# Performance work log

Hardware: AMD Instinct MI355X
Metric: run time of the kernel (lower is better)

## Reference

```python
import jax, jax.numpy as jnp
import numpy as np

E, D, H, T = 8, 1024, 2048, 2048  # num_expert, d_model, d_hidden, tokens

def setup_inputs() -> dict:
    key = jax.random.key(0)
    ks = jax.random.split(key, 7)
    return {
        "moe_inp": jax.random.normal(ks[0], (T, D), jnp.float32),
        "Wg": jax.random.normal(ks[1], (D, E), jnp.float32) * 0.02,
        "bg": jnp.zeros((E,), jnp.float32),
        "W1": jax.random.normal(ks[2], (E, D, H), jnp.float32) * 0.02,
        "b1": jnp.zeros((E, H), jnp.float32),
        "W2": jax.random.normal(ks[3], (E, H, D), jnp.float32) * 0.02,
        "b2": jnp.zeros((E, D), jnp.float32),
        "top_k": 2,
    }

def reference(moe_inp, Wg, bg, W1, b1, W2, b2, top_k):
    # NaiveGate: linear gate, top-k select, softmax over the selected logits
    logits = moe_inp @ Wg + bg                      # [T, E]
    top_vals, top_idx = jax.lax.top_k(logits, top_k)  # [T, k]
    gate_score = jax.nn.softmax(top_vals, axis=-1)    # [T, k]

    # Exact (no capacity drop) MoE: scan over experts, mask-combine.
    # Equivalent math to scatter -> per-expert FFN -> gather -> bmm(gate_score, ...).
    def body(acc, xs):
        e, w1, bb1, w2, bb2 = xs
        h = jax.nn.gelu(moe_inp @ w1 + bb1)          # [T, H]
        y = h @ w2 + bb2                             # [T, D]
        w = jnp.sum(jnp.where(top_idx == e, gate_score, 0.0), axis=-1)  # [T]
        return acc + w[:, None] * y, None

    init = jnp.zeros_like(moe_inp)
    xs = (jnp.arange(E), W1, b1, W2, b2)
    moe_outp, _ = jax.lax.scan(body, init, xs)
    return moe_outp, top_idx
```

## Files before the change

### kernel.cpp

```cpp
#include <hip/hip_runtime.h>
#include <stdint.h>

#define T_TOK 2048
#define D_DIM 1024
#define H_DIM 2048
#define N_EXP 8
#define MAXS  4608

#define WS_CNT    0
#define WS_BTOK   256
#define WS_BW     (WS_BTOK + N_EXP*2048*4)
#define WS_XG     (WS_BW + N_EXP*2048*4)
#define WS_HBUF   (WS_XG + (size_t)MAXS*1024*2)
#define WS_W1T    (WS_HBUF + (size_t)MAXS*2048*2)
#define WS_W2T    (WS_W1T + (size_t)N_EXP*1024*2048*2)

typedef __bf16 bf16x8 __attribute__((ext_vector_type(8)));
typedef float  f32x4  __attribute__((ext_vector_type(4)));

__device__ __forceinline__ unsigned short f2bf(float f) {
  unsigned int u = __float_as_uint(f);
  u += 0x7fffu + ((u >> 16) & 1u);
  return (unsigned short)(u >> 16);
}

__device__ __forceinline__ float gelu_tanh(float x) {
  const float u = 0.7978845608028654f * (x + 0.044715f * x * x * x);
  const float t = __expf(-2.0f * fabsf(u));
  const float th = (1.0f - t) * __builtin_amdgcn_rcpf(1.0f + t);
  return 0.5f * x * (1.0f + copysignf(th, u));
}


__device__ __forceinline__ void transpose_body(const float* __restrict__ in,
                                               unsigned short* __restrict__ out,
                                               int Rout, int Cin, int tx, int ty,
                                               void* smem_) {
  float (*tile)[68] = (float (*)[68])smem_;
  const int c0 = tx * 64, r0 = ty * 64;
  const int tid = threadIdx.x;
#pragma unroll
  for (int p = 0; p < 4; ++p) {
    const int idx = p * 256 + tid;
    const int r = idx >> 4, c4 = idx & 15;
    *(float4*)&tile[r][c4 * 4] = *(const float4*)(in + (size_t)(r0 + r) * Cin + c0 + c4 * 4);
  }
  __syncthreads();
#pragma unroll
  for (int p = 0; p < 2; ++p) {
    const int idx = p * 256 + tid;
    const int oc = idx >> 3, seg = idx & 7;
    unsigned u[4];
#pragma unroll
    for (int j = 0; j < 4; ++j) {
      const unsigned lo = f2bf(tile[seg * 8 + 2 * j][oc]);
      const unsigned hi = f2bf(tile[seg * 8 + 2 * j + 1][oc]);
      u[j] = lo | (hi << 16);
    }
    *(uint4*)(out + (size_t)(c0 + oc) * Rout + r0 + seg * 8) = make_uint4(u[0], u[1], u[2], u[3]);
  }
}

__device__ __forceinline__ void gate_body(int t, const float* __restrict__ x,
                                          const float* __restrict__ Wg,
                                          const float* __restrict__ bg,
                                          float* __restrict__ out_idx,
                                          int* __restrict__ cnt, int* __restrict__ btok,
                                          float* __restrict__ bw) {
  const int lane = threadIdx.x & 63;
  float p[8];
#pragma unroll
  for (int i = 0; i < 8; ++i) p[i] = 0.f;
  const float* xr = x + (size_t)t * D_DIM;
  for (int i = lane; i < D_DIM; i += 64) {
    const float xv = xr[i];
    const float4 wa = ((const float4*)(Wg + i * 8))[0];
    const float4 wb = ((const float4*)(Wg + i * 8))[1];
    p[0] += xv * wa.x; p[1] += xv * wa.y; p[2] += xv * wa.z; p[3] += xv * wa.w;
    p[4] += xv * wb.x; p[5] += xv * wb.y; p[6] += xv * wb.z; p[7] += xv * wb.w;
  }
#pragma unroll
  for (int off = 32; off > 0; off >>= 1) {
#pragma unroll
    for (int i = 0; i < 8; ++i) p[i] += __shfl_xor(p[i], off);
  }
  if (lane == 0) {
#pragma unroll
    for (int i = 0; i < 8; ++i) p[i] += bg[i];
    int i0 = 0; float v0 = p[0];
#pragma unroll
    for (int i = 1; i < 8; ++i) if (p[i] > v0) { v0 = p[i]; i0 = i; }
    int i1 = -1; float v1 = -3.4e38f;
#pragma unroll
    for (int i = 0; i < 8; ++i) if (i != i0 && p[i] > v1) { v1 = p[i]; i1 = i; }
    const float ex = expf(v1 - v0);
    const float inv = 1.f / (1.f + ex);
    out_idx[t * 2 + 0] = (float)i0;
    out_idx[t * 2 + 1] = (float)i1;
    int s0 = atomicAdd(&cnt[i0], 1);
    btok[i0 * 2048 + s0] = t; bw[i0 * 2048 + s0] = inv;
    int s1 = atomicAdd(&cnt[i1], 1);
    btok[i1 * 2048 + s1] = t; bw[i1 * 2048 + s1] = ex * inv;
  }
}

__device__ __forceinline__ void expert_seg(const int* __restrict__ cnt, int e,
                                           int& base, int& ce, int& pcnt, int& total) {
  int off = 0; base = 0; ce = 0; pcnt = 0;
#pragma unroll
  for (int i = 0; i < N_EXP; ++i) {
    const int c = cnt[i];
    const int p = (c + 63) & ~63;
    if (i == e) { base = off; ce = c; pcnt = p; }
    off += p;
  }
  total = off;
}

template <int MODE>
__device__ __forceinline__ void gemm_body(
    int lin, const unsigned short* __restrict__ A, const unsigned short* __restrict__ B,
    const float* __restrict__ bias, const int* __restrict__ cnt,
    const int* __restrict__ btok, const float* __restrict__ bw,
    unsigned short* __restrict__ Hout, float* __restrict__ out, void* smem_) {
  constexpr int K   = (MODE == 0) ? D_DIM : H_DIM;
  constexpr int SK  = (MODE == 0) ? 1 : 2;
  constexpr int KS  = K / SK;
  constexpr int NIT = KS / 32;

  const int glo = lin & 7;
  const int mt  = (lin >> 3) & 31;
  const int g   = ((lin >> 8) << 3) | glo;
  int nt, e, ksl;
  if (MODE == 0) { nt = g & 15; e = g >> 4; ksl = 0; }
  else           { nt = g & 7;  e = (g >> 3) & 7; ksl = g >> 6; }

  int base, ce, pcnt, total;
  expert_seg(cnt, e, base, ce, pcnt, total);
  if (mt * 64 >= pcnt) return;
  const int row0 = base + mt * 64;
  const int n0 = nt * 128;

  unsigned short (*As)[64 * 32] = (unsigned short (*)[64 * 32])smem_;
  unsigned short (*Bs)[128 * 32] = (unsigned short (*)[128 * 32])((char*)smem_ + 8192);

  const int tid = threadIdx.x;
  const int lane = tid & 63;
  const int wv = tid >> 6;
  const int wm = wv >> 1;
  const int wn = wv & 1;

  const unsigned short* Ab = A + (size_t)row0 * K + ksl * KS;
  const unsigned short* Bb = B + (size_t)e * ((size_t)H_DIM * D_DIM) + (size_t)n0 * K + ksl * KS;

  f32x4 acc[2][4];
#pragma unroll
  for (int i = 0; i < 2; ++i)
#pragma unroll
    for (int j = 0; j < 4; ++j) acc[i][j] = (f32x4)(0.0f);

  const int subr = lane >> 2;
  const int ks = (lane & 3) * 8;
  const int fr = lane & 15;
  const int kq = (lane >> 4) * 8;

  auto stage = [&](int kt, int b) {
    const int k0 = kt * 32;
    {
      const int r = wv * 16 + subr;
      const unsigned short* ga = Ab + (size_t)r * K + (k0 + ks);
      __builtin_amdgcn_global_load_lds(
          (__attribute__((address_space(1))) void*)ga,
          (__attribute__((address_space(3))) void*)(As[b] + wv * 16 * 32), 16, 0, 0);
    }
#pragma unroll
    for (int it = 0; it < 2; ++it) {
      const int ci = wv + it * 4;
      const int r = ci * 16 + subr;
      const unsigned short* gb = Bb + (size_t)r * K + (k0 + ks);
      __builtin_amdgcn_global_load_lds(
          (__attribute__((address_space(1))) void*)gb,
          (__attribute__((address_space(3))) void*)(Bs[b] + ci * 16 * 32), 16, 0, 0);
    }
  };

  stage(0, 0);
  for (int i = 0; i < NIT; ++i) {
    const int b = i & 1;
    __syncthreads();
    if (i + 1 < NIT) stage(i + 1, b ^ 1);
    bf16x8 av[2], bv[4];
#pragma unroll
    for (int mi = 0; mi < 2; ++mi)
      av[mi] = *(const bf16x8*)(As[b] + (wm * 32 + mi * 16 + fr) * 32 + kq);
#pragma unroll
    for (int ni = 0; ni < 4; ++ni)
      bv[ni] = *(const bf16x8*)(Bs[b] + (wn * 64 + ni * 16 + fr) * 32 + kq);
#pragma unroll
    for (int mi = 0; mi < 2; ++mi)
#pragma unroll
      for (int ni = 0; ni < 4; ++ni)
        acc[mi][ni] = __builtin_amdgcn_mfma_f32_16x16x32_bf16(av[mi], bv[ni], acc[mi][ni], 0, 0, 0);
  }

  if (MODE == 0) {
    const float* bb = bias + (size_t)e * H_DIM + n0;
#pragma unroll
    for (int mi = 0; mi < 2; ++mi) {
      const int rb = wm * 32 + mi * 16 + (lane >> 4) * 4;
#pragma unroll
      for (int r = 0; r < 4; ++r) {
        unsigned short* hp = Hout + (size_t)(row0 + rb + r) * H_DIM + n0;
#pragma unroll
        for (int ni = 0; ni < 4; ++ni) {
          const int col = wn * 64 + ni * 16 + fr;
          hp[col] = f2bf(gelu_tanh(acc[mi][ni][r] + bb[col]));
        }
      }
    }
  } else {
    const float* bb = bias + (size_t)e * D_DIM + n0;
#pragma unroll
    for (int mi = 0; mi < 2; ++mi) {
      const int rb = wm * 32 + mi * 16 + (lane >> 4) * 4;
#pragma unroll
      for (int r = 0; r < 4; ++r) {
        const int local = mt * 64 + rb + r;
        if (local < ce) {
          const int tok = btok[e * 2048 + local];
          const float w = bw[e * 2048 + local];
          float* op = out + (size_t)tok * D_DIM + n0;
#pragma unroll
          for (int ni = 0; ni < 4; ++ni) {
            const int col = wn * 64 + ni * 16 + fr;
            const float bias_once = (ksl == 0) ? bb[col] : 0.f;
            atomicAdd(op + col, w * (acc[mi][ni][r] + bias_once));
          }
        }
      }
    }
  }
}


__global__ void __launch_bounds__(256) prep_kernel(
    const float* __restrict__ x, const float* __restrict__ Wg,
    const float* __restrict__ bg, const float* __restrict__ W1,
    float* __restrict__ out, int* __restrict__ cnt, int* __restrict__ btok,
    float* __restrict__ bw, unsigned short* __restrict__ W1t) {
  __shared__ __align__(16) char smem[17408];
  const int bid = blockIdx.x;
  if (bid < 2048) {
    ((float4*)out)[bid * 256 + threadIdx.x] = make_float4(0.f, 0.f, 0.f, 0.f);
  } else if (bid < 2560) {
    gate_body((bid - 2048) * 4 + (threadIdx.x >> 6), x, Wg, bg,
              out + (size_t)T_TOK * D_DIM, cnt, btok, bw);
  } else {
    const int lin = bid - 2560;
    const int e = lin >> 9, l9 = lin & 511;
    transpose_body(W1 + (size_t)e * (D_DIM * H_DIM), W1t + (size_t)e * (D_DIM * H_DIM),
                   D_DIM, H_DIM, l9 & 31, l9 >> 5, smem);
  }
}

__global__ void gather_cvt(const float* __restrict__ x, const int* __restrict__ cnt,
                           const int* __restrict__ btok, unsigned short* __restrict__ Xg) {
  const int s = blockIdx.x;
  int off = 0, e = -1, loc = 0, c_e = 0;
#pragma unroll
  for (int i = 0; i < N_EXP; ++i) {
    const int c = cnt[i];
    const int p = (c + 63) & ~63;
    if (e < 0 && s < off + p) { e = i; loc = s - off; c_e = c; }
    off += p;
  }
  if (e < 0) return;
  uint2* orow = (uint2*)(Xg + (size_t)s * D_DIM);
  if (loc < c_e) {
    const int t = btok[e * 2048 + loc];
    const float4 v = ((const float4*)(x + (size_t)t * D_DIM))[threadIdx.x];
    uint2 u;
    u.x = (unsigned)f2bf(v.x) | ((unsigned)f2bf(v.y) << 16);
    u.y = (unsigned)f2bf(v.z) | ((unsigned)f2bf(v.w) << 16);
    orow[threadIdx.x] = u;
  } else {
    orow[threadIdx.x] = make_uint2(0u, 0u);
  }
}

__global__ void __launch_bounds__(256) gemm0_w2t(
    const unsigned short* __restrict__ Xg, const unsigned short* __restrict__ W1t,
    const float* __restrict__ b1, const int* __restrict__ cnt,
    const int* __restrict__ btok, const float* __restrict__ bw,
    unsigned short* __restrict__ Hbuf, const float* __restrict__ W2,
    unsigned short* __restrict__ W2t) {
  __shared__ __align__(16) char smem[24576];
  if (blockIdx.x < 4096) {
    gemm_body<0>(blockIdx.x, Xg, W1t, b1, cnt, btok, bw, Hbuf, nullptr, smem);
  } else {
    const int lin = blockIdx.x - 4096;
    const int e = lin >> 9, l9 = lin & 511;
    transpose_body(W2 + (size_t)e * (D_DIM * H_DIM), W2t + (size_t)e * (D_DIM * H_DIM),
                   H_DIM, D_DIM, l9 & 15, l9 >> 4, smem);
  }
}

__global__ void __launch_bounds__(256) moe_gemm1(
    const unsigned short* __restrict__ Hbuf, const unsigned short* __restrict__ W2t,
    const float* __restrict__ b2, const int* __restrict__ cnt,
    const int* __restrict__ btok, const float* __restrict__ bw,
    float* __restrict__ out) {
  __shared__ __align__(16) char smem[24576];
  gemm_body<1>(blockIdx.x, Hbuf, W2t, b2, cnt, btok, bw, nullptr, out, smem);
}

extern "C" void kernel_launch(void* const* d_in, const int* in_sizes, int n_in,
                              void* d_out, int out_size, void* d_ws, size_t ws_size,
                              hipStream_t stream) {
  const float* moe_inp = (const float*)d_in[0];
  const float* Wg = (const float*)d_in[1];
  const float* bg = (const float*)d_in[2];
  const float* W1 = (const float*)d_in[3];
  const float* b1 = (const float*)d_in[4];
  const float* W2 = (const float*)d_in[5];
  const float* b2 = (const float*)d_in[6];
  float* out = (float*)d_out;

  char* ws = (char*)d_ws;
  int* cnt  = (int*)(ws + WS_CNT);
  int* btok = (int*)(ws + WS_BTOK);
  float* bw = (float*)(ws + WS_BW);
  unsigned short* Xg   = (unsigned short*)(ws + WS_XG);
  unsigned short* Hbuf = (unsigned short*)(ws + WS_HBUF);
  unsigned short* W1t  = (unsigned short*)(ws + WS_W1T);
  unsigned short* W2t  = (unsigned short*)(ws + WS_W2T);

  hipMemsetAsync(cnt, 0, 256, stream);
  prep_kernel<<<dim3(6656), dim3(256), 0, stream>>>(moe_inp, Wg, bg, W1,
                                                    out, cnt, btok, bw, W1t);
  gather_cvt<<<dim3(MAXS), dim3(256), 0, stream>>>(moe_inp, cnt, btok, Xg);
  gemm0_w2t<<<dim3(8192), dim3(256), 0, stream>>>(Xg, W1t, b1, cnt, btok, bw,
                                                  Hbuf, W2, W2t);
  moe_gemm1<<<dim3(4096), dim3(256), 0, stream>>>(Hbuf, W2t, b2, cnt, btok, bw, out);
}
```

Before: 318.5 us.

## Fuse token gather and bf16 conversion into first expert GEMM A-loading

Removes the separate gather_cvt kernel. The first GEMM now loads fp32 token rows directly through btok indices into registers, converts them to bf16 and writes them into LDS, with register prefetch of the next k-tile overlapping the MFMA work. This saves a launch and a full write and read of the gathered bf16 buffer, at the cost of twice the fp32 A-traffic per tile and repeated conversion across the 16 N-tiles. The transpose helper is also restructured to batch global loads before the LDS writes.

Result: no change. 319.7 us (+0.4%).

```diff
diff --git a/kernel.cpp b/kernel.cpp
--- a/kernel.cpp
+++ b/kernel.cpp
@@ -39,25 +39,38 @@
   float (*tile)[68] = (float (*)[68])smem_;
   const int c0 = tx * 64, r0 = ty * 64;
   const int tid = threadIdx.x;
+  float4 v[4];
 #pragma unroll
   for (int p = 0; p < 4; ++p) {
     const int idx = p * 256 + tid;
     const int r = idx >> 4, c4 = idx & 15;
-    *(float4*)&tile[r][c4 * 4] = *(const float4*)(in + (size_t)(r0 + r) * Cin + c0 + c4 * 4);
+    v[p] = *(const float4*)(in + (size_t)(r0 + r) * Cin + c0 + c4 * 4);
+  }
+#pragma unroll
+  for (int p = 0; p < 4; ++p) {
+    const int idx = p * 256 + tid;
+    const int r = idx >> 4, c4 = idx & 15;
+    *(float4*)&tile[r][c4 * 4] = v[p];
   }
   __syncthreads();
+  unsigned u[2][4];
 #pragma unroll
   for (int p = 0; p < 2; ++p) {
     const int idx = p * 256 + tid;
     const int oc = idx >> 3, seg = idx & 7;
-    unsigned u[4];
 #pragma unroll
     for (int j = 0; j < 4; ++j) {
       const unsigned lo = f2bf(tile[seg * 8 + 2 * j][oc]);
       const unsigned hi = f2bf(tile[seg * 8 + 2 * j + 1][oc]);
-      u[j] = lo | (hi << 16);
-    }
-    *(uint4*)(out + (size_t)(c0 + oc) * Rout + r0 + seg * 8) = make_uint4(u[0], u[1], u[2], u[3]);
+      u[p][j] = lo | (hi << 16);
+    }
+  }
+#pragma unroll
+  for (int p = 0; p < 2; ++p) {
+    const int idx = p * 256 + tid;
+    const int oc = idx >> 3, seg = idx & 7;
+    *(uint4*)(out + (size_t)(c0 + oc) * Rout + r0 + seg * 8) =
+        make_uint4(u[p][0], u[p][1], u[p][2], u[p][3]);
   }
 }
 
@@ -119,7 +132,8 @@
 
 template <int MODE>
 __device__ __forceinline__ void gemm_body(
-    int lin, const unsigned short* __restrict__ A, const unsigned short* __restrict__ B,
+    int lin, const float* __restrict__ X, const unsigned short* __restrict__ A,
+    const unsigned short* __restrict__ B,
     const float* __restrict__ bias, const int* __restrict__ cnt,
     const int* __restrict__ btok, const float* __restrict__ bw,
     unsigned short* __restrict__ Hout, float* __restrict__ out, void* smem_) {
@@ -150,7 +164,6 @@
   const int wm = wv >> 1;
   const int wn = wv & 1;
 
-  const unsigned short* Ab = A + (size_t)row0 * K + ksl * KS;
   const unsigned short* Bb = B + (size_t)e * ((size_t)H_DIM * D_DIM) + (size_t)n0 * K + ksl * KS;
 
   f32x4 acc[2][4];
@@ -160,15 +173,49 @@
     for (int j = 0; j < 4; ++j) acc[i][j] = (f32x4)(0.0f);
 
   const int subr = lane >> 2;
-  const int ks = (lane & 3) * 8;
+  const int ksf = (lane & 3) * 8;
   const int fr = lane & 15;
   const int kq = (lane >> 4) * 8;
 
+  const unsigned short* Ab = nullptr;
+  const float* a_src = nullptr;
+  bool a_real = false;
+  if constexpr (MODE == 0) {
+    const int al = mt * 64 + wv * 16 + subr;
+    a_real = (al < ce);
+    const int tok = a_real ? btok[e * 2048 + al] : 0;
+    a_src = X + (size_t)tok * D_DIM + ksf;
+  } else {
+    Ab = A + (size_t)row0 * K + ksl * KS;
+  }
+
+  float4 pa0, pa1;
+  auto stageA_load = [&](int kt) {
+    if constexpr (MODE == 0) {
+      if (a_real) {
+        pa0 = *(const float4*)(a_src + kt * 32);
+        pa1 = *(const float4*)(a_src + kt * 32 + 4);
+      } else {
+        pa0 = make_float4(0.f, 0.f, 0.f, 0.f);
+        pa1 = make_float4(0.f, 0.f, 0.f, 0.f);
+      }
+    }
+  };
+  auto stageA_write = [&](int b) {
+    if constexpr (MODE == 0) {
+      uint4 u;
+      u.x = (unsigned)f2bf(pa0.x) | ((unsigned)f2bf(pa0.y) << 16);
+      u.y = (unsigned)f2bf(pa0.z) | ((unsigned)f2bf(pa0.w) << 16);
+      u.z = (unsigned)f2bf(pa1.x) | ((unsigned)f2bf(pa1.y) << 16);
+      u.w = (unsigned)f2bf(pa1.z) | ((unsigned)f2bf(pa1.w) << 16);
+      *(uint4*)(As[b] + (wv * 16 + subr) * 32 + ksf) = u;
+    }
+  };
   auto stage = [&](int kt, int b) {
     const int k0 = kt * 32;
-    {
+    if constexpr (MODE == 1) {
       const int r = wv * 16 + subr;
-      const unsigned short* ga = Ab + (size_t)r * K + (k0 + ks);
+      const unsigned short* ga = Ab + (size_t)r * K + (k0 + ksf);
       __builtin_amdgcn_global_load_lds(
           (__attribute__((address_space(1))) void*)ga,
           (__attribute__((address_space(3))) void*)(As[b] + wv * 16 * 32), 16, 0, 0);
@@ -177,18 +224,20 @@
     for (int it = 0; it < 2; ++it) {
       const int ci = wv + it * 4;
       const int r = ci * 16 + subr;
-      const unsigned short* gb = Bb + (size_t)r * K + (k0 + ks);
+      const unsigned short* gb = Bb + (size_t)r * K + (k0 + ksf);
       __builtin_amdgcn_global_load_lds(
           (__attribute__((address_space(1))) void*)gb,
           (__attribute__((address_space(3))) void*)(Bs[b] + ci * 16 * 32), 16, 0, 0);
     }
   };
 
+  stageA_load(0);
   stage(0, 0);
+  stageA_write(0);
   for (int i = 0; i < NIT; ++i) {
     const int b = i & 1;
     __syncthreads();
-    if (i + 1 < NIT) stage(i + 1, b ^ 1);
+    if (i + 1 < NIT) { stageA_load(i + 1); stage(i + 1, b ^ 1); }
     bf16x8 av[2], bv[4];
 #pragma unroll
     for (int mi = 0; mi < 2; ++mi)
@@ -201,6 +250,7 @@
 #pragma unroll
       for (int ni = 0; ni < 4; ++ni)
         acc[mi][ni] = __builtin_amdgcn_mfma_f32_16x16x32_bf16(av[mi], bv[ni], acc[mi][ni], 0, 0, 0);
+    if (i + 1 < NIT) stageA_write(b ^ 1);
   }
 
   if (MODE == 0) {
@@ -263,40 +313,15 @@
   }
 }
 
-__global__ void gather_cvt(const float* __restrict__ x, const int* __restrict__ cnt,
-                           const int* __restrict__ btok, unsigned short* __restrict__ Xg) {
-  const int s = blockIdx.x;
-  int off = 0, e = -1, loc = 0, c_e = 0;
-#pragma unroll
-  for (int i = 0; i < N_EXP; ++i) {
-    const int c = cnt[i];
-    const int p = (c + 63) & ~63;
-    if (e < 0 && s < off + p) { e = i; loc = s - off; c_e = c; }
-    off += p;
-  }
-  if (e < 0) return;
-  uint2* orow = (uint2*)(Xg + (size_t)s * D_DIM);
-  if (loc < c_e) {
-    const int t = btok[e * 2048 + loc];
-    const float4 v = ((const float4*)(x + (size_t)t * D_DIM))[threadIdx.x];
-    uint2 u;
-    u.x = (unsigned)f2bf(v.x) | ((unsigned)f2bf(v.y) << 16);
-    u.y = (unsigned)f2bf(v.z) | ((unsigned)f2bf(v.w) << 16);
-    orow[threadIdx.x] = u;
-  } else {
-    orow[threadIdx.x] = make_uint2(0u, 0u);
-  }
-}
-
 __global__ void __launch_bounds__(256) gemm0_w2t(
-    const unsigned short* __restrict__ Xg, const unsigned short* __restrict__ W1t,
+    const float* __restrict__ x, const unsigned short* __restrict__ W1t,
     const float* __restrict__ b1, const int* __restrict__ cnt,
     const int* __restrict__ btok, const float* __restrict__ bw,
     unsigned short* __restrict__ Hbuf, const float* __restrict__ W2,
     unsigned short* __restrict__ W2t) {
   __shared__ __align__(16) char smem[24576];
   if (blockIdx.x < 4096) {
-    gemm_body<0>(blockIdx.x, Xg, W1t, b1, cnt, btok, bw, Hbuf, nullptr, smem);
+    gemm_body<0>(blockIdx.x, x, nullptr, W1t, b1, cnt, btok, bw, Hbuf, nullptr, smem);
   } else {
     const int lin = blockIdx.x - 4096;
     const int e = lin >> 9, l9 = lin & 511;
@@ -311,7 +336,7 @@
     const int* __restrict__ btok, const float* __restrict__ bw,
     float* __restrict__ out) {
   __shared__ __align__(16) char smem[24576];
-  gemm_body<1>(blockIdx.x, Hbuf, W2t, b2, cnt, btok, bw, nullptr, out, smem);
+  gemm_body<1>(blockIdx.x, nullptr, Hbuf, W2t, b2, cnt, btok, bw, nullptr, out, smem);
 }
 
 extern "C" void kernel_launch(void* const* d_in, const int* in_sizes, int n_in,
@@ -330,7 +355,6 @@
   int* cnt  = (int*)(ws + WS_CNT);
   int* btok = (int*)(ws + WS_BTOK);
   float* bw = (float*)(ws + WS_BW);
-  unsigned short* Xg   = (unsigned short*)(ws + WS_XG);
   unsigned short* Hbuf = (unsigned short*)(ws + WS_HBUF);
   unsigned short* W1t  = (unsigned short*)(ws + WS_W1T);
   unsigned short* W2t  = (unsigned short*)(ws + WS_W2T);
@@ -338,8 +362,7 @@
   hipMemsetAsync(cnt, 0, 256, stream);
   prep_kernel<<<dim3(6656), dim3(256), 0, stream>>>(moe_inp, Wg, bg, W1,
                                                     out, cnt, btok, bw, W1t);
-  gather_cvt<<<dim3(MAXS), dim3(256), 0, stream>>>(moe_inp, cnt, btok, Xg);
-  gemm0_w2t<<<dim3(8192), dim3(256), 0, stream>>>(Xg, W1t, b1, cnt, btok, bw,
+  gemm0_w2t<<<dim3(8192), dim3(256), 0, stream>>>(moe_inp, W1t, b1, cnt, btok, bw,
                                                   Hbuf, W2, W2t);
   moe_gemm1<<<dim3(4096), dim3(256), 0, stream>>>(Hbuf, W2t, b2, cnt, btok, bw, out);
 }
```
